# Performance work log

Measured on AMD Instinct MI355X. Metric: run time of the kernel, lower is better.

Reference implementation:

```python
import jax, jax.numpy as jnp
import numpy as np

HEADS = 12
DIM_HEAD = 64
SCALE = DIM_HEAD ** -0.5


def setup_inputs() -> dict:
    key = jax.random.key(0)
    ks = jax.random.split(key, 7)
    b, n, dim = 16, 1024, 768
    inner = HEADS * DIM_HEAD
    x = jax.random.normal(ks[0], (b, n, dim), dtype=jnp.float32)
    Wq = jax.random.normal(ks[1], (dim, inner), dtype=jnp.float32) * (dim ** -0.5)
    Wkv = jax.random.normal(ks[2], (dim, 2 * inner), dtype=jnp.float32) * (dim ** -0.5)
    mix_pre = jax.random.normal(ks[3], (HEADS, HEADS), dtype=jnp.float32)
    mix_post = jax.random.normal(ks[4], (HEADS, HEADS), dtype=jnp.float32)
    Wo = jax.random.normal(ks[5], (inner, dim), dtype=jnp.float32) * (inner ** -0.5)
    bo = jnp.zeros((dim,), dtype=jnp.float32)
    return {"x": x, "Wq": Wq, "Wkv": Wkv, "mix_pre": mix_pre,
            "mix_post": mix_post, "Wo": Wo, "bo": bo}


def reference(x, Wq, Wkv, mix_pre, mix_post, Wo, bo):
    b, n, dim = x.shape
    h, d = HEADS, DIM_HEAD
    # projections (context is None -> context = x)
    q = (x @ Wq).reshape(b, n, h, d).transpose(0, 2, 1, 3)        # b h n d
    kv = x @ Wkv
    k = kv[..., : h * d].reshape(b, n, h, d).transpose(0, 2, 1, 3)
    v = kv[..., h * d:].reshape(b, n, h, d).transpose(0, 2, 1, 3)
    # scaled QK^T
    attn = jnp.einsum('bhid,bhjd->bhij', q, k) * SCALE             # b h n n
    # talking-heads pre-softmax: mix over head dim
    attn = jnp.einsum('bhij,hg->bgij', attn, mix_pre)
    attn = jax.nn.softmax(attn, axis=-1)
    # talking-heads post-softmax
    attn = jnp.einsum('bhij,hg->bgij', attn, mix_post)
    out = jnp.einsum('bhij,bhjd->bhid', attn, v)                   # b h n d
    out = out.transpose(0, 2, 1, 3).reshape(b, n, h * d)           # b n (h d)
    return out @ Wo + bo
```

## Files before the change

### kernel.cpp

```cpp
#include <hip/hip_runtime.h>


typedef _Float16 f16;
typedef _Float16 f16x8 __attribute__((ext_vector_type(8)));
typedef _Float16 f16x4 __attribute__((ext_vector_type(4)));
typedef float f32x4 __attribute__((ext_vector_type(4)));
typedef float fv4 __attribute__((ext_vector_type(4)));

#define MFMA(a, b, c) __builtin_amdgcn_mfma_f32_16x16x32_f16(a, b, c, 0, 0, 0)

__global__ __launch_bounds__(256) void k_cast_x(const float* __restrict__ x,
                                                f16* __restrict__ xb) {
  int idx = (blockIdx.x * 256 + threadIdx.x) * 8;
  fv4 a = *(const fv4*)(x + idx);
  fv4 b = *(const fv4*)(x + idx + 4);
  f16x8 o;
  o[0] = (f16)a[0]; o[1] = (f16)a[1]; o[2] = (f16)a[2]; o[3] = (f16)a[3];
  o[4] = (f16)b[0]; o[5] = (f16)b[1]; o[6] = (f16)b[2]; o[7] = (f16)b[3];
  *(f16x8*)(xb + idx) = o;
}

__global__ __launch_bounds__(256) void k_prep_w(const float* __restrict__ Wq,
                                                const float* __restrict__ Wkv,
                                                const float* __restrict__ Wo,
                                                f16* __restrict__ Wt,
                                                f16* __restrict__ WoT) {
  int idx = blockIdx.x * 256 + threadIdx.x;
  if (idx < 2304 * 768) {
    int n = idx / 768, k = idx % 768;
    float v = (n < 768) ? Wq[k * 768 + n] * 0.125f
                        : Wkv[k * 1536 + (n - 768)];
    Wt[idx] = (f16)v;
  } else {
    int id2 = idx - 2304 * 768;
    int n = id2 / 768, k = id2 % 768;
    WoT[id2] = (f16)Wo[k * 768 + n];
  }
}

__global__ __launch_bounds__(256) void k_gemm_qkv(const f16* __restrict__ A,
                                                  const f16* __restrict__ Bt,
                                                  f16* __restrict__ qb,
                                                  f16* __restrict__ kb,
                                                  f16* __restrict__ vb) {
  __shared__ f16 As[128 * 72];
  __shared__ f16 Bs[128 * 72];
  const int tid = threadIdx.x;
  const int m0 = blockIdx.y << 7;
  const int n0 = blockIdx.x << 7;
  const int lane = tid & 63, w = tid >> 6;
  const int quad = lane >> 4, col = lane & 15;
  const int wm = (w >> 1) << 6, wn = (w & 1) << 6;
  const f32x4 z4 = {0.f, 0.f, 0.f, 0.f};
  f32x4 acc[4][4];
#pragma unroll
  for (int i = 0; i < 4; ++i)
#pragma unroll
    for (int j = 0; j < 4; ++j) acc[i][j] = z4;

  for (int k0 = 0; k0 < 768; k0 += 64) {
#pragma unroll
    for (int s = 0; s < 4; ++s) {
      int u = s * 256 + tid;
      int row = u >> 3, seg = (u & 7) << 3;
      *(f16x8*)&As[row * 72 + seg] = *(const f16x8*)(A + (m0 + row) * 768 + k0 + seg);
      *(f16x8*)&Bs[row * 72 + seg] = *(const f16x8*)(Bt + (n0 + row) * 768 + k0 + seg);
    }
    __syncthreads();
#pragma unroll
    for (int kk = 0; kk < 64; kk += 32) {
      f16x8 af[4], bf[4];
#pragma unroll
      for (int ic = 0; ic < 4; ++ic)
        af[ic] = *(f16x8*)&As[(wm + ic * 16 + col) * 72 + kk + quad * 8];
#pragma unroll
      for (int jc = 0; jc < 4; ++jc)
        bf[jc] = *(f16x8*)&Bs[(wn + jc * 16 + col) * 72 + kk + quad * 8];
#pragma unroll
      for (int ic = 0; ic < 4; ++ic)
#pragma unroll
        for (int jc = 0; jc < 4; ++jc) acc[ic][jc] = MFMA(af[ic], bf[jc], acc[ic][jc]);
    }
    __syncthreads();
  }
#pragma unroll
  for (int jc = 0; jc < 4; ++jc) {
    int gn = n0 + wn + jc * 16 + col;
#pragma unroll
    for (int ic = 0; ic < 4; ++ic)
#pragma unroll
      for (int r = 0; r < 4; ++r) {
        int gm = m0 + wm + ic * 16 + (quad << 2) + r;
        int b = gm >> 10, i = gm & 1023;
        f16 v = (f16)acc[ic][jc][r];
        if (gn < 768) {
          int h = gn >> 6, dd = gn & 63;
          qb[(((b * 12 + h) << 10) + i) * 64 + dd] = v;
        } else if (gn < 1536) {
          int t = gn - 768; int h = t >> 6, dd = t & 63;
          kb[(((b * 12 + h) << 10) + i) * 64 + dd] = v;
        } else {
          int t = gn - 1536; int h = t >> 6, dd = t & 63;
          vb[(((b * 12 + h) << 10) + i) * 64 + dd] = v;
        }
      }
  }
}

__global__ __launch_bounds__(256) void k_transpose_v(const f16* __restrict__ vb,
                                                     f16* __restrict__ vt) {
  __shared__ f16 t[64 * 72];
  const int bh = blockIdx.x;
  const int n0 = blockIdx.y << 6;
  const int tid = threadIdx.x;
#pragma unroll
  for (int s = 0; s < 2; ++s) {
    int u = s * 256 + tid;
    int r = u >> 3, c = (u & 7) << 3;
    *(f16x8*)&t[r * 72 + c] = *(const f16x8*)(vb + (bh * 1024 + n0 + r) * 64 + c);
  }
  __syncthreads();
#pragma unroll
  for (int s = 0; s < 2; ++s) {
    int u = s * 256 + tid;
    int d = u >> 3, c = (u & 7) << 3;
    f16x8 o;
#pragma unroll
    for (int e = 0; e < 8; ++e) o[e] = t[(c + e) * 72 + d];
    *(f16x8*)(vt + (bh * 64 + d) * 1024 + n0 + c) = o;
  }
}

__global__ __launch_bounds__(256, 2) void k_attn(
    const f16* __restrict__ qb, const f16* __restrict__ kb, const f16* __restrict__ vt,
    const float* __restrict__ mixp, const float* __restrict__ mixq,
    f16* __restrict__ ob) {
  __shared__ f16 Blds[512 * 40];
  __shared__ f16 Pm[16 * 16 * 40];
  __shared__ float m_s[256];
  __shared__ float l_s[256];

  const int tid = threadIdx.x;
  const int bid = blockIdx.x;
  const int b = bid >> 6;
  const int i0 = (bid & 63) << 4;
  const int lane = tid & 63;
  const int w = tid >> 6;
  const int quad = lane >> 4, col = lane & 15;
  const int q4 = quad << 2;
  const int w3 = w * 3, w8 = w * 8, w4 = w << 2;

  {
    f16x8 z8;
#pragma unroll
    for (int e = 0; e < 8; ++e) z8[e] = (f16)0.f;
#pragma unroll
    for (int u = 0; u < 10; ++u) *(f16x8*)&Blds[(tid + u * 256) * 8] = z8;
  }

  f16x8 b_pre, b_post;
#pragma unroll
  for (int e = 0; e < 8; ++e) {
    int hk = quad * 8 + e;
    bool ok = (hk < 12) && (col < 12);
    b_pre[e]  = ok ? (f16)mixp[hk * 12 + col] : (f16)0.f;
    b_post[e] = ok ? (f16)mixq[hk * 12 + col] : (f16)0.f;
  }

  f16x8 qf[3][2];
#pragma unroll
  for (int h3 = 0; h3 < 3; ++h3)
#pragma unroll
    for (int kc = 0; kc < 2; ++kc)
      qf[h3][kc] = *(const f16x8*)(qb + (((b * 12 + w3 + h3) << 10) + i0 + col) * 64 +
                                   kc * 32 + quad * 8);
  __syncthreads();

  auto computeS = [&](int j0, f32x4 (&d1)[8]) {
    const f32x4 z4 = {0.f, 0.f, 0.f, 0.f};
    f32x4 s[3][2];
#pragma unroll
    for (int h3 = 0; h3 < 3; ++h3) {
      s[h3][0] = z4; s[h3][1] = z4;
      const f16* kbase = kb + (((b * 12 + w3 + h3) << 10) + j0) * 64;
#pragma unroll
      for (int js = 0; js < 2; ++js)
#pragma unroll
        for (int kc = 0; kc < 2; ++kc) {
          f16x8 kf = *(const f16x8*)(kbase + (js * 16 + col) * 64 + kc * 32 + quad * 8);
          s[h3][js] = MFMA(qf[h3][kc], kf, s[h3][js]);
        }
    }
#pragma unroll
    for (int h3 = 0; h3 < 3; ++h3)
#pragma unroll
      for (int js = 0; js < 2; ++js)
#pragma unroll
        for (int r = 0; r < 4; ++r)
          Blds[(((q4 + r) << 5) + js * 16 + col) * 40 + w3 + h3] = (f16)s[h3][js][r];
    __syncthreads();
#pragma unroll
    for (int u = 0; u < 8; ++u) {
      f16x8 sf = *(f16x8*)&Blds[((w8 + u) * 16 + col) * 40 + quad * 8];
      d1[u] = MFMA(sf, b_pre, z4);
    }
  };

  float m_run[4], l_run[4];
#pragma unroll
  for (int ii = 0; ii < 4; ++ii) { m_run[ii] = -1e30f; l_run[ii] = 0.f; }

  for (int j0 = 0; j0 < 1024; j0 += 32) {
    f32x4 d1[8];
    computeS(j0, d1);
#pragma unroll
    for (int ii = 0; ii < 4; ++ii) {
      float mx = -1e30f;
#pragma unroll
      for (int uu = 0; uu < 2; ++uu)
#pragma unroll
        for (int r = 0; r < 4; ++r) mx = fmaxf(mx, d1[ii * 2 + uu][r]);
      mx = fmaxf(mx, __shfl_xor(mx, 16));
      mx = fmaxf(mx, __shfl_xor(mx, 32));
      float mnew = fmaxf(m_run[ii], mx);
      float se = 0.f;
#pragma unroll
      for (int uu = 0; uu < 2; ++uu)
#pragma unroll
        for (int r = 0; r < 4; ++r) se += __expf(d1[ii * 2 + uu][r] - mnew);
      se += __shfl_xor(se, 16);
      se += __shfl_xor(se, 32);
      l_run[ii] = l_run[ii] * __expf(m_run[ii] - mnew) + se;
      m_run[ii] = mnew;
    }
    __syncthreads();
  }
  if (quad == 0) {
#pragma unroll
    for (int ii = 0; ii < 4; ++ii) {
      m_s[col * 16 + w4 + ii] = m_run[ii];
      l_s[col * 16 + w4 + ii] = l_run[ii];
    }
  }
  __syncthreads();

  float mv[4], il[4];
#pragma unroll
  for (int ii = 0; ii < 4; ++ii) {
    mv[ii] = m_s[col * 16 + w4 + ii];
    il[ii] = 1.f / l_s[col * 16 + w4 + ii];
  }

  f32x4 oa[3][4];
  {
    const f32x4 z4 = {0.f, 0.f, 0.f, 0.f};
#pragma unroll
    for (int g = 0; g < 3; ++g)
#pragma unroll
      for (int dc = 0; dc < 4; ++dc) oa[g][dc] = z4;
  }

  for (int j0 = 0; j0 < 1024; j0 += 32) {
    f32x4 d1[8];
    computeS(j0, d1);
#pragma unroll
    for (int u = 0; u < 8; ++u) {
      int c0 = (w8 + u) * 16;
      int ii = u >> 1;
#pragma unroll
      for (int r = 0; r < 4; ++r) {
        float P = __expf(d1[u][r] - mv[ii]) * il[ii];
        Blds[(c0 + q4 + r) * 40 + col] = (f16)P;
      }
    }
    f32x4 d2[8];
    {
      const f32x4 z4 = {0.f, 0.f, 0.f, 0.f};
#pragma unroll
      for (int u = 0; u < 8; ++u) {
        f16x8 pf = *(f16x8*)&Blds[((w8 + u) * 16 + col) * 40 + quad * 8];
        d2[u] = MFMA(pf, b_post, z4);
      }
    }
#pragma unroll
    for (int u = 0; u < 8; ++u) {
      int iloc = (w8 + u) >> 1;
      int jbase = ((u & 1) << 4) + q4;
      f16x4 pk;
#pragma unroll
      for (int r = 0; r < 4; ++r) pk[r] = (f16)d2[u][r];
      *(f16x4*)&Pm[(col * 16 + iloc) * 40 + jbase] = pk;
    }
    __syncthreads();
#pragma unroll
    for (int gg = 0; gg < 3; ++gg) {
      int gp = w3 + gg;
      f16x8 af = *(f16x8*)&Pm[(gp * 16 + col) * 40 + quad * 8];
#pragma unroll
      for (int dc = 0; dc < 4; ++dc) {
        f16x8 vf = *(const f16x8*)(vt + (((b * 12 + gp) * 64 + dc * 16 + col) << 10) +
                                   j0 + quad * 8);
        oa[gg][dc] = MFMA(af, vf, oa[gg][dc]);
      }
    }
    __syncthreads();
  }

#pragma unroll
  for (int gg = 0; gg < 3; ++gg) {
    int gp = w3 + gg;
#pragma unroll
    for (int dc = 0; dc < 4; ++dc)
#pragma unroll
      for (int r = 0; r < 4; ++r)
        ob[((b << 10) + i0 + q4 + r) * 768 + gp * 64 + dc * 16 + col] =
            (f16)oa[gg][dc][r];
  }
}

__global__ __launch_bounds__(256) void k_gemm_out(const f16* __restrict__ A,
                                                  const f16* __restrict__ Bt,
                                                  const float* __restrict__ bias,
                                                  float* __restrict__ out) {
  __shared__ f16 As[128 * 72];
  __shared__ f16 Bs[128 * 72];
  const int tid = threadIdx.x;
  const int m0 = blockIdx.y << 7;
  const int n0 = blockIdx.x << 7;
  const int lane = tid & 63, w = tid >> 6;
  const int quad = lane >> 4, col = lane & 15;
  const int wm = (w >> 1) << 6, wn = (w & 1) << 6;
  const f32x4 z4 = {0.f, 0.f, 0.f, 0.f};
  f32x4 acc[4][4];
#pragma unroll
  for (int i = 0; i < 4; ++i)
#pragma unroll
    for (int j = 0; j < 4; ++j) acc[i][j] = z4;

  for (int k0 = 0; k0 < 768; k0 += 64) {
#pragma unroll
    for (int s = 0; s < 4; ++s) {
      int u = s * 256 + tid;
      int row = u >> 3, seg = (u & 7) << 3;
      *(f16x8*)&As[row * 72 + seg] = *(const f16x8*)(A + (m0 + row) * 768 + k0 + seg);
      *(f16x8*)&Bs[row * 72 + seg] = *(const f16x8*)(Bt + (n0 + row) * 768 + k0 + seg);
    }
    __syncthreads();
#pragma unroll
    for (int kk = 0; kk < 64; kk += 32) {
      f16x8 af[4], bf[4];
#pragma unroll
      for (int ic = 0; ic < 4; ++ic)
        af[ic] = *(f16x8*)&As[(wm + ic * 16 + col) * 72 + kk + quad * 8];
#pragma unroll
      for (int jc = 0; jc < 4; ++jc)
        bf[jc] = *(f16x8*)&Bs[(wn + jc * 16 + col) * 72 + kk + quad * 8];
#pragma unroll
      for (int ic = 0; ic < 4; ++ic)
#pragma unroll
        for (int jc = 0; jc < 4; ++jc) acc[ic][jc] = MFMA(af[ic], bf[jc], acc[ic][jc]);
    }
    __syncthreads();
  }
#pragma unroll
  for (int jc = 0; jc < 4; ++jc) {
    int gn = n0 + wn + jc * 16 + col;
    float bv = bias[gn];
#pragma unroll
    for (int ic = 0; ic < 4; ++ic)
#pragma unroll
      for (int r = 0; r < 4; ++r) {
        int gm = m0 + wm + ic * 16 + (quad << 2) + r;
        out[gm * 768 + gn] = acc[ic][jc][r] + bv;
      }
  }
}

extern "C" void kernel_launch(void* const* d_in, const int* in_sizes, int n_in,
                              void* d_out, int out_size, void* d_ws, size_t ws_size,
                              hipStream_t stream) {
  const float* x    = (const float*)d_in[0];
  const float* Wq   = (const float*)d_in[1];
  const float* Wkv  = (const float*)d_in[2];
  const float* mixp = (const float*)d_in[3];
  const float* mixq = (const float*)d_in[4];
  const float* Wo   = (const float*)d_in[5];
  const float* bo   = (const float*)d_in[6];
  float* out = (float*)d_out;

  char* ws = (char*)d_ws;
  f16* xb  = (f16*)(ws);
  f16* Wt  = (f16*)(ws + 25165824);
  f16* WoT = (f16*)(ws + 28704768);
  f16* qb  = (f16*)(ws + 29884416);
  f16* kb  = (f16*)(ws + 55050240);
  f16* vb  = (f16*)(ws + 80216064);
  f16* vt  = xb;
  f16* obuf = vb;

  k_cast_x<<<dim3(6144), dim3(256), 0, stream>>>(x, xb);
  k_prep_w<<<dim3(9216), dim3(256), 0, stream>>>(Wq, Wkv, Wo, Wt, WoT);
  k_gemm_qkv<<<dim3(18, 128), dim3(256), 0, stream>>>(xb, Wt, qb, kb, vb);
  k_transpose_v<<<dim3(192, 16), dim3(256), 0, stream>>>(vb, vt);
  k_attn<<<dim3(1024), dim3(256), 0, stream>>>(qb, kb, vt, mixp, mixq, obuf);
  k_gemm_out<<<dim3(6, 128), dim3(256), 0, stream>>>(obuf, WoT, bo, out);
}
```

Measured before the change: 786.3 us.

## Restructure talking-heads attention kernel with swizzled LDS layouts and 16x16x16 head-mix MFMAs

Rewrites the attention kernel's shared-memory layout using XOR-swizzled, padded buffers. The 12-head mixing now uses the smaller 16x16x16 MFMA with a K=16 padded operand instead of K=32. The mix_pre matrix is pre-scaled by log2(e) so softmax can use native exp2. Each wave keeps per-lane partial max and sum statistics without cross-lane shuffles and merges them across waves at the end. The first pass double-buffers LDS to drop one barrier per iteration, and occupancy is raised to 3 blocks per CU, which risks register pressure or spills.

New measurement: 1.379 ms. 75.4% more time.

```diff
diff --git a/kernel.cpp b/kernel.cpp
--- a/kernel.cpp
+++ b/kernel.cpp
@@ -2,12 +2,15 @@
 
 
 typedef _Float16 f16;
+typedef _Float16 f16x2 __attribute__((ext_vector_type(2)));
+typedef _Float16 f16x4 __attribute__((ext_vector_type(4)));
 typedef _Float16 f16x8 __attribute__((ext_vector_type(8)));
-typedef _Float16 f16x4 __attribute__((ext_vector_type(4)));
 typedef float f32x4 __attribute__((ext_vector_type(4)));
 typedef float fv4 __attribute__((ext_vector_type(4)));
 
-#define MFMA(a, b, c) __builtin_amdgcn_mfma_f32_16x16x32_f16(a, b, c, 0, 0, 0)
+#define MFMA32(a, b, c) __builtin_amdgcn_mfma_f32_16x16x32_f16(a, b, c, 0, 0, 0)
+#define MFMA16(a, b, c) __builtin_amdgcn_mfma_f32_16x16x16f16(a, b, c, 0, 0, 0)
+#define EXP2(x) __builtin_amdgcn_exp2f(x)
 
 __global__ __launch_bounds__(256) void k_cast_x(const float* __restrict__ x,
                                                 f16* __restrict__ xb) {
@@ -79,7 +82,7 @@
 #pragma unroll
       for (int ic = 0; ic < 4; ++ic)
 #pragma unroll
-        for (int jc = 0; jc < 4; ++jc) acc[ic][jc] = MFMA(af[ic], bf[jc], acc[ic][jc]);
+        for (int jc = 0; jc < 4; ++jc) acc[ic][jc] = MFMA32(af[ic], bf[jc], acc[ic][jc]);
     }
     __syncthreads();
   }
@@ -131,40 +134,43 @@
   }
 }
 
-__global__ __launch_bounds__(256, 2) void k_attn(
+__global__ __launch_bounds__(256, 3) void k_attn(
     const f16* __restrict__ qb, const f16* __restrict__ kb, const f16* __restrict__ vt,
     const float* __restrict__ mixp, const float* __restrict__ mixq,
     f16* __restrict__ ob) {
-  __shared__ f16 Blds[512 * 40];
-  __shared__ f16 Pm[16 * 16 * 40];
-  __shared__ float m_s[256];
-  __shared__ float l_s[256];
+  __shared__ f16 SA[10368];
+  __shared__ f16 SB[10368];
+  __shared__ float msL[1024];
+  __shared__ float lsL[1024];
 
   const int tid = threadIdx.x;
   const int bid = blockIdx.x;
-  const int b = bid >> 6;
+  const int b  = bid >> 6;
   const int i0 = (bid & 63) << 4;
   const int lane = tid & 63;
   const int w = tid >> 6;
   const int quad = lane >> 4, col = lane & 15;
   const int q4 = quad << 2;
-  const int w3 = w * 3, w8 = w * 8, w4 = w << 2;
+  const int w3 = w * 3;
+  const int sp0   = (w & 1) ? 1 : 0;
+  const int soloS = (w & 1) ? 0 : 2;
+  const int pairH = w3 + sp0;
+  const int soloH = w3 + soloS;
+  const f32x4 z4 = {0.f, 0.f, 0.f, 0.f};
 
   {
-    f16x8 z8;
-#pragma unroll
-    for (int e = 0; e < 8; ++e) z8[e] = (f16)0.f;
-#pragma unroll
-    for (int u = 0; u < 10; ++u) *(f16x8*)&Blds[(tid + u * 256) * 8] = z8;
-  }
-
-  f16x8 b_pre, b_post;
-#pragma unroll
-  for (int e = 0; e < 8; ++e) {
-    int hk = quad * 8 + e;
-    bool ok = (hk < 12) && (col < 12);
-    b_pre[e]  = ok ? (f16)mixp[hk * 12 + col] : (f16)0.f;
-    b_post[e] = ok ? (f16)mixq[hk * 12 + col] : (f16)0.f;
+    f16x8 z8 = {};
+    for (int z = tid; z < 1296; z += 256) ((f16x8*)SA)[z] = z8;
+    for (int z = tid; z < 1296; z += 256) ((f16x8*)SB)[z] = z8;
+  }
+
+  f16x4 b_pre, b_post;
+#pragma unroll
+  for (int e = 0; e < 4; ++e) {
+    int k = q4 + e;
+    bool ok = (k < 12) && (col < 12);
+    b_pre[e]  = ok ? (f16)(mixp[k * 12 + col] * 1.44269504f) : (f16)0.f;
+    b_post[e] = ok ? (f16)(mixq[k * 12 + col]) : (f16)0.f;
   }
 
   f16x8 qf[3][2];
@@ -176,145 +182,146 @@
                                    kc * 32 + quad * 8);
   __syncthreads();
 
-  auto computeS = [&](int j0, f32x4 (&d1)[8]) {
-    const f32x4 z4 = {0.f, 0.f, 0.f, 0.f};
+  const int granP = (((pairH >> 2) ^ quad) << 2) + (pairH & 3);
+  const int granS = (((soloH >> 2) ^ quad) << 2) + (soloH & 3);
+  const int mixOff = (quad ^ (col >> 2)) << 2;
+
+  auto computeS = [&](int j0, f16* Sbuf) {
     f32x4 s[3][2];
 #pragma unroll
     for (int h3 = 0; h3 < 3; ++h3) {
-      s[h3][0] = z4; s[h3][1] = z4;
       const f16* kbase = kb + (((b * 12 + w3 + h3) << 10) + j0) * 64;
 #pragma unroll
-      for (int js = 0; js < 2; ++js)
+      for (int jn = 0; jn < 2; ++jn) {
+        f32x4 acc = z4;
 #pragma unroll
         for (int kc = 0; kc < 2; ++kc) {
-          f16x8 kf = *(const f16x8*)(kbase + (js * 16 + col) * 64 + kc * 32 + quad * 8);
-          s[h3][js] = MFMA(qf[h3][kc], kf, s[h3][js]);
+          f16x8 kf = *(const f16x8*)(kbase + (jn * 16 + col) * 64 + kc * 32 + quad * 8);
+          acc = MFMA32(qf[h3][kc], kf, acc);
         }
-    }
-#pragma unroll
-    for (int h3 = 0; h3 < 3; ++h3)
-#pragma unroll
-      for (int js = 0; js < 2; ++js)
+        s[h3][jn] = acc;
+      }
+    }
+#pragma unroll
+    for (int jn = 0; jn < 2; ++jn) {
+      int base2 = (jn * 16 + col) * 324 + q4 * 20;
+#pragma unroll
+      for (int r = 0; r < 4; ++r) {
+        int b2 = base2 + r * 20;
+        f16x2 pk; pk[0] = (f16)s[sp0][jn][r]; pk[1] = (f16)s[sp0 + 1][jn][r];
+        *(f16x2*)&Sbuf[b2 + granP] = pk;
+        Sbuf[b2 + granS] = (f16)s[soloS][jn][r];
+      }
+    }
+  };
+
+  float m_run[4], l_run[4];
+#pragma unroll
+  for (int r = 0; r < 4; ++r) { m_run[r] = -1e30f; l_run[r] = 0.f; }
+
+  for (int t = 0; t < 32; ++t) {
+    f16* Sbuf = (t & 1) ? SB : SA;
+    computeS(t * 32, Sbuf);
+    __syncthreads();
+    f32x4 d1[8];
+#pragma unroll
+    for (int u = 0; u < 8; ++u) {
+      f16x4 sf = *(f16x4*)&Sbuf[(w * 8 + u) * 324 + col * 20 + mixOff];
+      d1[u] = MFMA16(sf, b_pre, z4);
+    }
+#pragma unroll
+    for (int r = 0; r < 4; ++r) {
+      float mt = d1[0][r];
+#pragma unroll
+      for (int u = 1; u < 8; ++u) mt = fmaxf(mt, d1[u][r]);
+      float mnew = fmaxf(m_run[r], mt);
+      float se = 0.f;
+#pragma unroll
+      for (int u = 0; u < 8; ++u) se += EXP2(d1[u][r] - mnew);
+      l_run[r] = l_run[r] * EXP2(m_run[r] - mnew) + se;
+      m_run[r] = mnew;
+    }
+  }
+
+#pragma unroll
+  for (int r = 0; r < 4; ++r) {
+    msL[w * 256 + col * 16 + q4 + r] = m_run[r];
+    lsL[w * 256 + col * 16 + q4 + r] = l_run[r];
+  }
+  __syncthreads();
+  float mv[4], il[4];
+#pragma unroll
+  for (int r = 0; r < 4; ++r) {
+    int ix = col * 16 + q4 + r;
+    float M = msL[ix];
+    M = fmaxf(M, msL[256 + ix]);
+    M = fmaxf(M, msL[512 + ix]);
+    M = fmaxf(M, msL[768 + ix]);
+    float L = 0.f;
+#pragma unroll
+    for (int wp = 0; wp < 4; ++wp)
+      L += lsL[wp * 256 + ix] * EXP2(msL[wp * 256 + ix] - M);
+    mv[r] = M; il[r] = 1.f / L;
+  }
+
+  f32x4 oa[3][4];
+#pragma unroll
+  for (int g3 = 0; g3 < 3; ++g3)
+#pragma unroll
+    for (int dc = 0; dc < 4; ++dc) oa[g3][dc] = z4;
+
+  for (int t = 0; t < 32; ++t) {
+    const int j0 = t * 32;
+    computeS(j0, SA);
+    __syncthreads();
+#pragma unroll
+    for (int u = 0; u < 8; ++u) {
+      int v = w * 8 + u;
+      f16x4 sf = *(f16x4*)&SA[v * 324 + col * 20 + mixOff];
+      f32x4 d1 = MFMA16(sf, b_pre, z4);
+      if (col < 12) {
+        int pbase = v * 324 + q4 * 20 + (((col >> 2) ^ quad) << 2) + (col & 3);
 #pragma unroll
         for (int r = 0; r < 4; ++r)
-          Blds[(((q4 + r) << 5) + js * 16 + col) * 40 + w3 + h3] = (f16)s[h3][js][r];
+          SB[pbase + r * 20] = (f16)(EXP2(d1[r] - mv[r]) * il[r]);
+      }
+    }
     __syncthreads();
 #pragma unroll
     for (int u = 0; u < 8; ++u) {
-      f16x8 sf = *(f16x8*)&Blds[((w8 + u) * 16 + col) * 40 + quad * 8];
-      d1[u] = MFMA(sf, b_pre, z4);
-    }
-  };
-
-  float m_run[4], l_run[4];
-#pragma unroll
-  for (int ii = 0; ii < 4; ++ii) { m_run[ii] = -1e30f; l_run[ii] = 0.f; }
-
-  for (int j0 = 0; j0 < 1024; j0 += 32) {
-    f32x4 d1[8];
-    computeS(j0, d1);
-#pragma unroll
-    for (int ii = 0; ii < 4; ++ii) {
-      float mx = -1e30f;
-#pragma unroll
-      for (int uu = 0; uu < 2; ++uu)
-#pragma unroll
-        for (int r = 0; r < 4; ++r) mx = fmaxf(mx, d1[ii * 2 + uu][r]);
-      mx = fmaxf(mx, __shfl_xor(mx, 16));
-      mx = fmaxf(mx, __shfl_xor(mx, 32));
-      float mnew = fmaxf(m_run[ii], mx);
-      float se = 0.f;
-#pragma unroll
-      for (int uu = 0; uu < 2; ++uu)
-#pragma unroll
-        for (int r = 0; r < 4; ++r) se += __expf(d1[ii * 2 + uu][r] - mnew);
-      se += __shfl_xor(se, 16);
-      se += __shfl_xor(se, 32);
-      l_run[ii] = l_run[ii] * __expf(m_run[ii] - mnew) + se;
-      m_run[ii] = mnew;
-    }
-    __syncthreads();
-  }
-  if (quad == 0) {
-#pragma unroll
-    for (int ii = 0; ii < 4; ++ii) {
-      m_s[col * 16 + w4 + ii] = m_run[ii];
-      l_s[col * 16 + w4 + ii] = l_run[ii];
-    }
-  }
-  __syncthreads();
-
-  float mv[4], il[4];
-#pragma unroll
-  for (int ii = 0; ii < 4; ++ii) {
-    mv[ii] = m_s[col * 16 + w4 + ii];
-    il[ii] = 1.f / l_s[col * 16 + w4 + ii];
-  }
-
-  f32x4 oa[3][4];
-  {
-    const f32x4 z4 = {0.f, 0.f, 0.f, 0.f};
-#pragma unroll
-    for (int g = 0; g < 3; ++g)
-#pragma unroll
-      for (int dc = 0; dc < 4; ++dc) oa[g][dc] = z4;
-  }
-
-  for (int j0 = 0; j0 < 1024; j0 += 32) {
-    f32x4 d1[8];
-    computeS(j0, d1);
-#pragma unroll
-    for (int u = 0; u < 8; ++u) {
-      int c0 = (w8 + u) * 16;
-      int ii = u >> 1;
-#pragma unroll
-      for (int r = 0; r < 4; ++r) {
-        float P = __expf(d1[u][r] - mv[ii]) * il[ii];
-        Blds[(c0 + q4 + r) * 40 + col] = (f16)P;
-      }
-    }
-    f32x4 d2[8];
-    {
-      const f32x4 z4 = {0.f, 0.f, 0.f, 0.f};
-#pragma unroll
-      for (int u = 0; u < 8; ++u) {
-        f16x8 pf = *(f16x8*)&Blds[((w8 + u) * 16 + col) * 40 + quad * 8];
-        d2[u] = MFMA(pf, b_post, z4);
-      }
-    }
-#pragma unroll
-    for (int u = 0; u < 8; ++u) {
-      int iloc = (w8 + u) >> 1;
-      int jbase = ((u & 1) << 4) + q4;
-      f16x4 pk;
-#pragma unroll
-      for (int r = 0; r < 4; ++r) pk[r] = (f16)d2[u][r];
-      *(f16x4*)&Pm[(col * 16 + iloc) * 40 + jbase] = pk;
-    }
-    __syncthreads();
-#pragma unroll
-    for (int gg = 0; gg < 3; ++gg) {
-      int gp = w3 + gg;
-      f16x8 af = *(f16x8*)&Pm[(gp * 16 + col) * 40 + quad * 8];
+      int v = w * 8 + u;
+      f16x4 pf = *(f16x4*)&SB[v * 324 + col * 20 + mixOff];
+      f32x4 d2 = MFMA16(pf, b_post, z4);
+      if (col < 12) {
+#pragma unroll
+        for (int r = 0; r < 4; ++r)
+          SA[col * 648 + (q4 + r) * 40 + ((w ^ r) << 3) + u] = (f16)d2[r];
+      }
+    }
+    __syncthreads();
+#pragma unroll
+    for (int g3 = 0; g3 < 3; ++g3) {
+      int gp = w3 + g3;
+      f16x8 af = *(f16x8*)&SA[gp * 648 + col * 40 + ((quad ^ (col & 3)) << 3)];
 #pragma unroll
       for (int dc = 0; dc < 4; ++dc) {
         f16x8 vf = *(const f16x8*)(vt + (((b * 12 + gp) * 64 + dc * 16 + col) << 10) +
                                    j0 + quad * 8);
-        oa[gg][dc] = MFMA(af, vf, oa[gg][dc]);
-      }
-    }
-    __syncthreads();
-  }
-
-#pragma unroll
-  for (int gg = 0; gg < 3; ++gg) {
-    int gp = w3 + gg;
+        oa[g3][dc] = MFMA32(af, vf, oa[g3][dc]);
+      }
+    }
+    __syncthreads();
+  }
+
+#pragma unroll
+  for (int g3 = 0; g3 < 3; ++g3) {
+    int gp = w3 + g3;
 #pragma unroll
     for (int dc = 0; dc < 4; ++dc)
 #pragma unroll
       for (int r = 0; r < 4; ++r)
         ob[((b << 10) + i0 + q4 + r) * 768 + gp * 64 + dc * 16 + col] =
-            (f16)oa[gg][dc][r];
+            (f16)oa[g3][dc][r];
   }
 }
 
@@ -358,7 +365,7 @@
 #pragma unroll
       for (int ic = 0; ic < 4; ++ic)
 #pragma unroll
-        for (int jc = 0; jc < 4; ++jc) acc[ic][jc] = MFMA(af[ic], bf[jc], acc[ic][jc]);
+        for (int jc = 0; jc < 4; ++jc) acc[ic][jc] = MFMA32(af[ic], bf[jc], acc[ic][jc]);
     }
     __syncthreads();
   }
```
